# Performance work log

Measured on AMD Instinct MI355X. Metric: run time of the kernel, lower is better.

## Reference

```python
import jax, jax.numpy as jnp
import numpy as np

B, T, N_EMBED, HEADSIZE = 16, 2048, 1024, 128


def setup_inputs() -> dict:
    key = jax.random.key(0)
    kx, kq, kk, kv = jax.random.split(key, 4)
    x = jax.random.normal(kx, (B, T, N_EMBED), dtype=jnp.float32)
    # nn.Linear(n_embed, headsize, bias=False): y = x @ W, W stored [n_embed, headsize]
    s = (1.0 / np.sqrt(N_EMBED)).astype(np.float32)
    Wq = jax.random.normal(kq, (N_EMBED, HEADSIZE), dtype=jnp.float32) * s
    Wk = jax.random.normal(kk, (N_EMBED, HEADSIZE), dtype=jnp.float32) * s
    Wv = jax.random.normal(kv, (N_EMBED, HEADSIZE), dtype=jnp.float32) * s
    return {"x": x, "Wq": Wq, "Wk": Wk, "Wv": Wv}


def reference(x, Wq, Wk, Wv):
    Bsz, Tlen, C = x.shape
    q = x @ Wq  # [B, T, H]
    k = x @ Wk  # [B, T, H]
    v = x @ Wv  # [B, T, H]
    scale = C ** (-0.5)  # NOTE: original scales by n_embed**-0.5, not headsize**-0.5
    wt = jnp.einsum('bqh,bkh->bqk', q, k) * scale  # [B, T, T]
    causal = jnp.tril(jnp.ones((Tlen, Tlen), dtype=bool))
    wt = jnp.where(causal, wt, -jnp.inf)
    wt = jax.nn.softmax(wt, axis=-1)
    # dropout is identity in eval mode
    out = jnp.einsum('bqk,bkh->bqh', wt, v)  # [B, T, H]
    return out
```

## Files before the change

kernel.cpp:

```cpp
#include <hip/hip_runtime.h>
#include <hip/hip_bf16.h>

#define BATCH 16
#define TLEN 2048
#define CDIM 1024
#define HDIM 128

typedef __attribute__((ext_vector_type(8))) short bf16x8;
typedef __attribute__((ext_vector_type(4))) float f32x4;
typedef __attribute__((ext_vector_type(16))) float f32x16;
typedef __attribute__((ext_vector_type(4))) unsigned short u16x4;
typedef __attribute__((ext_vector_type(8))) unsigned short u16x8;

static __device__ __forceinline__ unsigned short f2bf(float f) {
    __hip_bfloat16 h = __float2bfloat16(f);
    return *(unsigned short*)&h;
}
static __device__ __forceinline__ unsigned pkbf(float a, float b) {
    return (unsigned)f2bf(a) | ((unsigned)f2bf(b) << 16);
}
static __device__ __forceinline__ int part_offs(int qc) {
    return qc + ((qc * qc - 2 * qc + (qc & 1)) >> 2);
}

typedef const __attribute__((address_space(1))) unsigned int* gas_t;
typedef __attribute__((address_space(3))) unsigned int* las_t;
static __device__ __forceinline__ void gl_lds16(const void* g, void* l) {
    __builtin_amdgcn_global_load_lds((gas_t)g, (las_t)l, 16, 0, 0);
}

__global__ __launch_bounds__(256) void pack_w(
    const float* __restrict__ Wq, const float* __restrict__ Wk,
    const float* __restrict__ Wv, unsigned short* __restrict__ wtb)
{
    const int which = blockIdx.y;
    const float* W = (which == 0) ? Wq : (which == 1) ? Wk : Wv;
    const int n = blockIdx.x >> 2;
    const int k = (blockIdx.x & 3) * 256 + threadIdx.x;
    wtb[((size_t)which * 128 + n) * 1024 + k] = f2bf(W[(size_t)k * 128 + n]);
}

__global__ __launch_bounds__(256, 2) void qkv_fused(
    const float* __restrict__ x, const unsigned short* __restrict__ wtb,
    unsigned short* __restrict__ qb, unsigned short* __restrict__ kb,
    unsigned short* __restrict__ vtb)
{
    __shared__ __align__(16) float          Axf[2][64 * 32];
    __shared__ __align__(16) unsigned short Bs[2][384 * 32];

    const int tid  = threadIdx.x;
    const int lane = tid & 63, wid = tid >> 6;
    const int c = lane & 15, g = lane >> 4;
    const int m0 = blockIdx.x * 64;

    f32x4 acc[4][6];
#pragma unroll
    for (int i = 0; i < 4; ++i)
#pragma unroll
        for (int j = 0; j < 6; ++j) acc[i][j] = (f32x4){0.f, 0.f, 0.f, 0.f};

#define STAGE(k0_, bi_)                                                      \
    { _Pragma("unroll")                                                      \
      for (int i_ = 0; i_ < 2; ++i_) {                                       \
          const int seg_ = wid * 2 + i_;                                     \
          const int row_ = seg_ * 8 + (lane >> 3);                           \
          const int col_ = (((lane & 7) ^ (row_ & 7)) << 2);                 \
          gl_lds16(x + (size_t)(m0 + row_) * CDIM + (k0_) + col_,            \
                   (char*)Axf[bi_] + seg_ * 1024);                           \
      }                                                                      \
      _Pragma("unroll")                                                      \
      for (int i_ = 0; i_ < 6; ++i_) {                                       \
          const int seg_ = wid * 6 + i_;                                     \
          const int row_ = seg_ * 16 + (lane >> 2);                          \
          const int col_ = (((lane & 3) ^ ((row_ >> 1) & 3)) << 3);          \
          gl_lds16(wtb + (size_t)row_ * 1024 + (k0_) + col_,                 \
                   (char*)Bs[bi_] + seg_ * 1024);                            \
      } }

    STAGE(0, 0);
    __syncthreads();

#pragma unroll 1
    for (int kt = 0; kt < 32; ++kt) {
        const int bi = kt & 1;
        if (kt < 31) STAGE((kt + 1) * 32, bi ^ 1);

        bf16x8 af[4], bf[6];
#pragma unroll
        for (int mf = 0; mf < 4; ++mf) {
            const int rm = mf * 16 + c;
            const char* base = (const char*)Axf[bi] + rm * 128;
            f32x4 lo = *(const f32x4*)(base + ((((2 * g)     ^ (rm & 7)) << 4)));
            f32x4 hi = *(const f32x4*)(base + ((((2 * g + 1) ^ (rm & 7)) << 4)));
            bf16x8 t;
            t[0] = f2bf(lo[0]); t[1] = f2bf(lo[1]); t[2] = f2bf(lo[2]); t[3] = f2bf(lo[3]);
            t[4] = f2bf(hi[0]); t[5] = f2bf(hi[1]); t[6] = f2bf(hi[2]); t[7] = f2bf(hi[3]);
            af[mf] = t;
        }
#pragma unroll
        for (int nf = 0; nf < 6; ++nf) {
            const int rn = wid * 96 + nf * 16 + c;
            bf[nf] = *(const bf16x8*)((const char*)Bs[bi] + rn * 64 +
                                      ((g ^ ((rn >> 1) & 3)) << 4));
        }

#pragma unroll
        for (int mf = 0; mf < 4; ++mf)
#pragma unroll
            for (int nf = 0; nf < 6; ++nf)
                acc[mf][nf] = __builtin_amdgcn_mfma_f32_16x16x32_bf16(
                    af[mf], bf[nf], acc[mf][nf], 0, 0, 0);

        __syncthreads();
    }

#pragma unroll
    for (int mf = 0; mf < 4; ++mf) {
#pragma unroll
        for (int nf = 0; nf < 6; ++nf) {
            const int col0 = wid * 96 + nf * 16;
            const int nt = col0 >> 7;
            const int nc = (col0 & 127) + c;
            const int m = m0 + mf * 16 + g * 4;
            if (nt == 0) {
#pragma unroll
                for (int r = 0; r < 4; ++r)
                    qb[(size_t)(m + r) * HDIM + nc] = f2bf(acc[mf][nf][r] * 0.03125f);
            } else if (nt == 1) {
#pragma unroll
                for (int r = 0; r < 4; ++r)
                    kb[(size_t)(m + r) * HDIM + nc] = f2bf(acc[mf][nf][r]);
            } else {
                const int b = m >> 11, tl = m & (TLEN - 1);
                u16x4 o;
                o[0] = f2bf(acc[mf][nf][0]); o[1] = f2bf(acc[mf][nf][1]);
                o[2] = f2bf(acc[mf][nf][2]); o[3] = f2bf(acc[mf][nf][3]);
                *(u16x4*)(vtb + ((size_t)b * HDIM + nc) * TLEN + tl) = o;
            }
        }
    }
#undef STAGE
}

__global__ __launch_bounds__(256, 2) void attn_partial(
    const short* __restrict__ qb, const short* __restrict__ kb,
    const short* __restrict__ vtb,
    unsigned short* __restrict__ Opart, float* __restrict__ mpart,
    float* __restrict__ lpart)
{
    const int kc = blockIdx.x;
    const int qc = blockIdx.y;
    const int b  = blockIdx.z;
    if (kc > (qc >> 1)) return;
    const int kv_base = kc * 256;
    const int qrel = qc * 128 - kv_base;
    int NT = ((qrel + 127) >> 6) + 1; if (NT > 4) NT = 4;

    __shared__ unsigned short Ks[2][64 * 128];
    __shared__ unsigned short Vs[2][128 * 64];

    const int tid  = threadIdx.x;
    const int wid  = tid >> 6;
    const int lane = tid & 63;
    const int c5 = lane & 31, hi = lane >> 5;
    const int q0w = qc * 128 + wid * 32;
    const int qg  = q0w + c5;
    const int pidx = b * 72 + part_offs(qc) + kc;

    const short* Kb  = kb  + (size_t)b * TLEN * HDIM;
    const short* Vtb = vtb + (size_t)b * HDIM * TLEN;

    bf16x8 qf[8];
#pragma unroll
    for (int ks = 0; ks < 8; ++ks)
        qf[ks] = *(const bf16x8*)(qb + ((size_t)b * TLEN + qg) * HDIM + ks * 16 + hi * 8);

    bf16x8 kst[4], vst[4];

#define GLOAD(kv0_)                                                          \
    {                                                                        \
        _Pragma("unroll")                                                    \
        for (int it = 0; it < 4; ++it) {                                     \
            const int o = tid * 16 + it * 4096;                              \
            const int kr = o >> 8, kcb = o & 0xF0;                           \
            kst[it] = *(const bf16x8*)((const char*)Kb +                     \
                        (size_t)((kv0_) + kr) * 256 + kcb);                  \
            const int vr = o >> 7, vcb = o & 0x70;                           \
            vst[it] = *(const bf16x8*)((const char*)Vtb +                    \
                        (size_t)vr * (TLEN * 2) + (size_t)(kv0_) * 2 + vcb); \
        }                                                                    \
    }
#define SSTORE(bi_)                                                          \
    {                                                                        \
        _Pragma("unroll")                                                    \
        for (int it = 0; it < 4; ++it) {                                     \
            const int o = tid * 16 + it * 4096;                              \
            const int kr = o >> 8, kcb = o & 0xF0;                           \
            *(bf16x8*)((char*)Ks[bi_] + kr * 256 + (kcb ^ ((kr & 7) << 4))) = kst[it]; \
            const int vr = o >> 7, vcb = o & 0x70;                           \
            *(bf16x8*)((char*)Vs[bi_] + vr * 128 + (vcb ^ ((vr & 7) << 4))) = vst[it]; \
        }                                                                    \
    }

    GLOAD(kv_base);
    SSTORE(0);
    __syncthreads();

    f32x16 oacc[4];
#pragma unroll
    for (int i = 0; i < 4; ++i)
#pragma unroll
        for (int r = 0; r < 16; ++r) oacc[i][r] = 0.f;
    float m_r = -1e30f;
    float l_r = 0.f;

#pragma unroll 1
    for (int t = 0; t < NT; ++t) {
        const int bi = t & 1;
        if (t + 1 < NT) GLOAD(kv_base + 64 * (t + 1));

        const int kv0 = kv_base + 64 * t;
        if (kv0 <= q0w + 31) {
            f32x16 s0, s1;
#pragma unroll
            for (int r = 0; r < 16; ++r) { s0[r] = 0.f; s1[r] = 0.f; }
            __builtin_amdgcn_s_setprio(1);
#pragma unroll
            for (int ks = 0; ks < 8; ++ks) {
                const int col = ks * 32 + hi * 16;
                const int off0 = c5 * 256 + (col ^ ((c5 & 7) << 4));
                const int off1 = (32 + c5) * 256 + (col ^ ((c5 & 7) << 4));
                bf16x8 a0 = *(const bf16x8*)((char*)Ks[bi] + off0);
                bf16x8 a1 = *(const bf16x8*)((char*)Ks[bi] + off1);
                s0 = __builtin_amdgcn_mfma_f32_32x32x16_bf16(a0, qf[ks], s0, 0, 0, 0);
                s1 = __builtin_amdgcn_mfma_f32_32x32x16_bf16(a1, qf[ks], s1, 0, 0, 0);
            }
            __builtin_amdgcn_s_setprio(0);

            if (kv0 + 63 > q0w) {
#pragma unroll
                for (int r = 0; r < 16; ++r) {
                    const int key0 = kv0 + (r & 3) + 8 * (r >> 2) + 4 * hi;
                    if (key0 > qg)      s0[r] = -INFINITY;
                    if (key0 + 32 > qg) s1[r] = -INFINITY;
                }
            }

            float t8[8];
#pragma unroll
            for (int i = 0; i < 8; ++i)
                t8[i] = fmaxf(fmaxf(s0[2*i], s0[2*i+1]), fmaxf(s1[2*i], s1[2*i+1]));
            float smax = fmaxf(fmaxf(fmaxf(t8[0], t8[1]), fmaxf(t8[2], t8[3])),
                               fmaxf(fmaxf(t8[4], t8[5]), fmaxf(t8[6], t8[7])));
            smax = fmaxf(smax, __shfl_xor(smax, 32));

            const bool defer = __all(smax - m_r <= 8.0f);
            const float mnew = defer ? m_r : fmaxf(m_r, smax);
            if (!defer) {
                const float alpha = __expf(m_r - mnew);
                l_r *= alpha;
#pragma unroll
                for (int hb = 0; hb < 4; ++hb) oacc[hb] = oacc[hb] * alpha;
            }
            m_r = mnew;

#pragma unroll
            for (int r = 0; r < 16; ++r) {
                s0[r] = __expf(s0[r] - mnew);
                s1[r] = __expf(s1[r] - mnew);
            }
            float a8[8];
#pragma unroll
            for (int i = 0; i < 8; ++i)
                a8[i] = (s0[2*i] + s0[2*i+1]) + (s1[2*i] + s1[2*i+1]);
            float psum = ((a8[0] + a8[1]) + (a8[2] + a8[3])) +
                         ((a8[4] + a8[5]) + (a8[6] + a8[7]));
            psum += __shfl_xor(psum, 32);
            l_r += psum;

            bf16x8 pa[4];
#pragma unroll
            for (int kb2 = 0; kb2 < 2; ++kb2) {
#pragma unroll
                for (int par = 0; par < 2; ++par) {
                    const int e = par * 8;
                    float v0, v1, v2, v3, v4, v5, v6, v7;
                    if (kb2 == 0) {
                        v0=s0[e+0]; v1=s0[e+1]; v2=s0[e+2]; v3=s0[e+3];
                        v4=s0[e+4]; v5=s0[e+5]; v6=s0[e+6]; v7=s0[e+7];
                    } else {
                        v0=s1[e+0]; v1=s1[e+1]; v2=s1[e+2]; v3=s1[e+3];
                        v4=s1[e+4]; v5=s1[e+5]; v6=s1[e+6]; v7=s1[e+7];
                    }
                    const unsigned w0 = pkbf(v0, v1), w1 = pkbf(v2, v3);
                    const unsigned w2 = pkbf(v4, v5), w3 = pkbf(v6, v7);
                    const unsigned X0 = hi ? w0 : w2;
                    const unsigned X1 = hi ? w1 : w3;
                    const unsigned R0 = (unsigned)__shfl_xor((int)X0, 32);
                    const unsigned R1 = (unsigned)__shfl_xor((int)X1, 32);
                    union { unsigned w[4]; bf16x8 v; } uu;
                    uu.w[0] = hi ? R0 : w0;  uu.w[1] = hi ? R1 : w1;
                    uu.w[2] = hi ? w2 : R0;  uu.w[3] = hi ? w3 : R1;
                    pa[kb2 * 2 + par] = uu.v;
                }
            }

            __builtin_amdgcn_s_setprio(1);
#pragma unroll
            for (int hb = 0; hb < 4; ++hb) {
                const int row = hb * 32 + c5;
#pragma unroll
                for (int ks = 0; ks < 4; ++ks) {
                    const int off = row * 128 + ((ks * 32 + hi * 16) ^ ((row & 7) << 4));
                    bf16x8 va = *(const bf16x8*)((char*)Vs[bi] + off);
                    oacc[hb] = __builtin_amdgcn_mfma_f32_32x32x16_bf16(va, pa[ks], oacc[hb], 0, 0, 0);
                }
            }
            __builtin_amdgcn_s_setprio(0);
        }

        if (t + 1 < NT) {
            SSTORE(bi ^ 1);
            __syncthreads();
        }
    }

    __syncthreads();
    char* sl = (char*)Ks + wid * 8192;
#pragma unroll
    for (int hb = 0; hb < 4; ++hb)
#pragma unroll
        for (int rq = 0; rq < 4; ++rq) {
            u16x4 o4;
            o4[0] = f2bf(oacc[hb][rq * 4 + 0]);
            o4[1] = f2bf(oacc[hb][rq * 4 + 1]);
            o4[2] = f2bf(oacc[hb][rq * 4 + 2]);
            o4[3] = f2bf(oacc[hb][rq * 4 + 3]);
            const int off = c5 * 256 + ((hb * 64 + rq * 16 + hi * 8) ^ ((c5 & 7) << 4));
            *(u16x4*)(sl + off) = o4;
        }
    asm volatile("s_waitcnt lgkmcnt(0)" ::: "memory");
    __builtin_amdgcn_sched_barrier(0);

    const int qr = lane >> 1, hf = lane & 1;
    unsigned short* Og = Opart + (size_t)pidx * 128 * 128 +
                         (size_t)(wid * 32 + qr) * 128 + hf * 64;
#pragma unroll
    for (int i = 0; i < 8; ++i) {
        const int off = qr * 256 + ((hf * 128 + i * 16) ^ ((qr & 7) << 4));
        *(u16x8*)(Og + i * 8) = *(const u16x8*)(sl + off);
    }
    if (hi == 0) {
        mpart[(size_t)pidx * 128 + wid * 32 + c5] = m_r;
        lpart[(size_t)pidx * 128 + wid * 32 + c5] = l_r;
    }
#undef GLOAD
#undef SSTORE
}

__global__ __launch_bounds__(256) void attn_combine(
    const unsigned short* __restrict__ Opart, const float* __restrict__ mpart,
    const float* __restrict__ lpart, float* __restrict__ out)
{
    const int qc = blockIdx.x;
    const int b  = blockIdx.y;
    const int n  = (qc >> 1) + 1;
    const int base = b * 72 + part_offs(qc);
    const int t   = threadIdx.x;
    const int row = t >> 1;
    const int d0  = (t & 1) * 64;

    float M = -INFINITY;
    for (int p = 0; p < n; ++p)
        M = fmaxf(M, mpart[(size_t)(base + p) * 128 + row]);
    float L = 0.f;
    for (int p = 0; p < n; ++p)
        L += __expf(mpart[(size_t)(base + p) * 128 + row] - M) *
             lpart[(size_t)(base + p) * 128 + row];

    float acc[64];
#pragma unroll
    for (int i = 0; i < 64; ++i) acc[i] = 0.f;

    for (int p = 0; p < n; ++p) {
        const float w = __expf(mpart[(size_t)(base + p) * 128 + row] - M);
        const bf16x8* src = (const bf16x8*)(Opart +
            ((size_t)(base + p) * 128 + row) * 128 + d0);
#pragma unroll
        for (int j = 0; j < 8; ++j) {
            bf16x8 v = src[j];
#pragma unroll
            for (int e = 0; e < 8; ++e) {
                union { unsigned u; float f; } x;
                x.u = ((unsigned)(unsigned short)v[e]) << 16;
                acc[j * 8 + e] += w * x.f;
            }
        }
    }

    const float invL = 1.f / L;
    float4* dst = (float4*)(out + ((size_t)(b * TLEN + qc * 128 + row)) * 128 + d0);
#pragma unroll
    for (int i = 0; i < 16; ++i)
        dst[i] = make_float4(acc[4*i] * invL, acc[4*i+1] * invL,
                             acc[4*i+2] * invL, acc[4*i+3] * invL);
}

extern "C" void kernel_launch(void* const* d_in, const int* in_sizes, int n_in,
                              void* d_out, int out_size, void* d_ws, size_t ws_size,
                              hipStream_t stream)
{
    const float* x  = (const float*)d_in[0];
    const float* Wq = (const float*)d_in[1];
    const float* Wk = (const float*)d_in[2];
    const float* Wv = (const float*)d_in[3];
    float* outp = (float*)d_out;

    const size_t per = (size_t)BATCH * TLEN * HDIM;
    unsigned short* qb  = (unsigned short*)d_ws;
    unsigned short* kb  = qb + per;
    unsigned short* vtb = kb + per;
    unsigned short* wtb = vtb + per;
    unsigned short* Opart = wtb + 384 * 1024;
    float* mpart = (float*)(Opart + (size_t)1152 * 128 * 128);
    float* lpart = mpart + (size_t)1152 * 128;

    dim3 gw(512, 3);
    pack_w<<<gw, 256, 0, stream>>>(Wq, Wk, Wv, wtb);

    qkv_fused<<<512, 256, 0, stream>>>(x, wtb, qb, kb, vtb);

    dim3 g2(8, 16, BATCH);
    attn_partial<<<g2, 256, 0, stream>>>((const short*)qb, (const short*)kb,
                                         (const short*)vtb, Opart, mpart, lpart);

    dim3 g3(16, BATCH);
    attn_combine<<<g3, 256, 0, stream>>>(Opart, mpart, lpart, outp);
}
```

Baseline: 133.9 us.

## Load QKV projection operands directly into registers instead of staging through LDS

The QKV projection GEMM no longer stages x and the weight tiles through double-buffered shared memory with global_load_lds and barriers. Each wave now loads its own A and B fragments straight from global memory into registers, using an even/odd register double buffer that overlaps the next K step's loads with the current MFMAs. This removes LDS traffic and the per-iteration __syncthreads. In exchange, the four waves each reload the shared x rows (4x redundant global/L2 reads), global accesses are less coalesced, and register pressure rises.

```diff
diff --git a/kernel.cpp b/kernel.cpp
--- a/kernel.cpp
+++ b/kernel.cpp
@@ -21,12 +21,6 @@
 }
 static __device__ __forceinline__ int part_offs(int qc) {
     return qc + ((qc * qc - 2 * qc + (qc & 1)) >> 2);
-}
-
-typedef const __attribute__((address_space(1))) unsigned int* gas_t;
-typedef __attribute__((address_space(3))) unsigned int* las_t;
-static __device__ __forceinline__ void gl_lds16(const void* g, void* l) {
-    __builtin_amdgcn_global_load_lds((gas_t)g, (las_t)l, 16, 0, 0);
 }
 
 __global__ __launch_bounds__(256) void pack_w(
@@ -45,73 +39,60 @@
     unsigned short* __restrict__ qb, unsigned short* __restrict__ kb,
     unsigned short* __restrict__ vtb)
 {
-    __shared__ __align__(16) float          Axf[2][64 * 32];
-    __shared__ __align__(16) unsigned short Bs[2][384 * 32];
-
     const int tid  = threadIdx.x;
     const int lane = tid & 63, wid = tid >> 6;
     const int c = lane & 15, g = lane >> 4;
     const int m0 = blockIdx.x * 64;
 
+    const float* xp = x + (size_t)(m0 + c) * CDIM + g * 8;
+    const unsigned short* wp = wtb + (size_t)(wid * 96 + c) * 1024 + g * 8;
+
     f32x4 acc[4][6];
 #pragma unroll
     for (int i = 0; i < 4; ++i)
 #pragma unroll
         for (int j = 0; j < 6; ++j) acc[i][j] = (f32x4){0.f, 0.f, 0.f, 0.f};
 
-#define STAGE(k0_, bi_)                                                      \
+    float4 Ae[8], Ao[8];
+    bf16x8 Be[6], Bo[6];
+
+#define LOADK(A_, B_, k0_)                                                   \
     { _Pragma("unroll")                                                      \
-      for (int i_ = 0; i_ < 2; ++i_) {                                       \
-          const int seg_ = wid * 2 + i_;                                     \
-          const int row_ = seg_ * 8 + (lane >> 3);                           \
-          const int col_ = (((lane & 7) ^ (row_ & 7)) << 2);                 \
-          gl_lds16(x + (size_t)(m0 + row_) * CDIM + (k0_) + col_,            \
-                   (char*)Axf[bi_] + seg_ * 1024);                           \
+      for (int mf_ = 0; mf_ < 4; ++mf_) {                                    \
+          const float* s_ = xp + (size_t)(mf_ * 16) * CDIM + (k0_);          \
+          A_[2 * mf_]     = *(const float4*)s_;                              \
+          A_[2 * mf_ + 1] = *(const float4*)(s_ + 4);                        \
       }                                                                      \
       _Pragma("unroll")                                                      \
-      for (int i_ = 0; i_ < 6; ++i_) {                                       \
-          const int seg_ = wid * 6 + i_;                                     \
-          const int row_ = seg_ * 16 + (lane >> 2);                          \
-          const int col_ = (((lane & 3) ^ ((row_ >> 1) & 3)) << 3);          \
-          gl_lds16(wtb + (size_t)row_ * 1024 + (k0_) + col_,                 \
-                   (char*)Bs[bi_] + seg_ * 1024);                            \
-      } }
-
-    STAGE(0, 0);
-    __syncthreads();
-
+      for (int nf_ = 0; nf_ < 6; ++nf_)                                      \
+          B_[nf_] = *(const bf16x8*)(wp + (size_t)(nf_ * 16) * 1024 + (k0_)); }
+
+#define COMPUTE(A_, B_)                                                      \
+    { bf16x8 af_[4];                                                         \
+      _Pragma("unroll")                                                      \
+      for (int mf_ = 0; mf_ < 4; ++mf_) {                                    \
+          const float4 lo_ = A_[2 * mf_], hi_ = A_[2 * mf_ + 1];             \
+          bf16x8 t_;                                                         \
+          t_[0] = f2bf(lo_.x); t_[1] = f2bf(lo_.y);                          \
+          t_[2] = f2bf(lo_.z); t_[3] = f2bf(lo_.w);                          \
+          t_[4] = f2bf(hi_.x); t_[5] = f2bf(hi_.y);                          \
+          t_[6] = f2bf(hi_.z); t_[7] = f2bf(hi_.w);                          \
+          af_[mf_] = t_;                                                     \
+      }                                                                      \
+      _Pragma("unroll")                                                      \
+      for (int mf_ = 0; mf_ < 4; ++mf_)                                      \
+          _Pragma("unroll")                                                  \
+          for (int nf_ = 0; nf_ < 6; ++nf_)                                  \
+              acc[mf_][nf_] = __builtin_amdgcn_mfma_f32_16x16x32_bf16(       \
+                  af_[mf_], B_[nf_], acc[mf_][nf_], 0, 0, 0); }
+
+    LOADK(Ae, Be, 0);
 #pragma unroll 1
-    for (int kt = 0; kt < 32; ++kt) {
-        const int bi = kt & 1;
-        if (kt < 31) STAGE((kt + 1) * 32, bi ^ 1);
-
-        bf16x8 af[4], bf[6];
-#pragma unroll
-        for (int mf = 0; mf < 4; ++mf) {
-            const int rm = mf * 16 + c;
-            const char* base = (const char*)Axf[bi] + rm * 128;
-            f32x4 lo = *(const f32x4*)(base + ((((2 * g)     ^ (rm & 7)) << 4)));
-            f32x4 hi = *(const f32x4*)(base + ((((2 * g + 1) ^ (rm & 7)) << 4)));
-            bf16x8 t;
-            t[0] = f2bf(lo[0]); t[1] = f2bf(lo[1]); t[2] = f2bf(lo[2]); t[3] = f2bf(lo[3]);
-            t[4] = f2bf(hi[0]); t[5] = f2bf(hi[1]); t[6] = f2bf(hi[2]); t[7] = f2bf(hi[3]);
-            af[mf] = t;
-        }
-#pragma unroll
-        for (int nf = 0; nf < 6; ++nf) {
-            const int rn = wid * 96 + nf * 16 + c;
-            bf[nf] = *(const bf16x8*)((const char*)Bs[bi] + rn * 64 +
-                                      ((g ^ ((rn >> 1) & 3)) << 4));
-        }
-
-#pragma unroll
-        for (int mf = 0; mf < 4; ++mf)
-#pragma unroll
-            for (int nf = 0; nf < 6; ++nf)
-                acc[mf][nf] = __builtin_amdgcn_mfma_f32_16x16x32_bf16(
-                    af[mf], bf[nf], acc[mf][nf], 0, 0, 0);
-
-        __syncthreads();
+    for (int kt = 0; kt < 32; kt += 2) {
+        LOADK(Ao, Bo, (kt + 1) * 32);
+        COMPUTE(Ae, Be);
+        if (kt + 2 < 32) LOADK(Ae, Be, (kt + 2) * 32);
+        COMPUTE(Ao, Bo);
     }
 
 #pragma unroll
@@ -139,7 +120,8 @@
             }
         }
     }
-#undef STAGE
+#undef LOADK
+#undef COMPUTE
 }
 
 __global__ __launch_bounds__(256, 2) void attn_partial(
```

Result: slower. 198.4 us (+48.2%).
